# Optimization experiments

Hardware: AMD Instinct MI355X
Metric: run time of the kernel (lower is better)

The kernel has to match this reference:

```python
import jax, jax.numpy as jnp
import numpy as np

DIM = 2048
MLP_MULT = 4
NUM_EXPERTS = 8
EXPERT_INTER = MLP_MULT * DIM // NUM_EXPERTS  # 1024
B, S = 4, 2048


def setup_inputs() -> dict:
    key = jax.random.key(0)
    k1, k2, k3, k4 = jax.random.split(key, 4)
    x = jax.random.normal(k1, (B, S, DIM), dtype=jnp.float32)
    expert_ids = jax.random.randint(k2, (B, S), 0, NUM_EXPERTS, dtype=jnp.int64)
    # kaiming-uniform-ish scale for gate_up; down_proj random (zeros in orig init
    # would make output trivially zero, unhelpful for a correctness baseline)
    bound_gu = float(np.sqrt(1.0 / DIM))
    gate_up_proj = jax.random.uniform(k3, (NUM_EXPERTS, DIM, 2 * EXPERT_INTER),
                                      dtype=jnp.float32, minval=-bound_gu, maxval=bound_gu)
    bound_dn = float(np.sqrt(1.0 / EXPERT_INTER))
    down_proj = jax.random.uniform(k4, (NUM_EXPERTS, EXPERT_INTER, DIM),
                                   dtype=jnp.float32, minval=-bound_dn, maxval=bound_dn)
    return {"x": x, "expert_ids": expert_ids,
            "gate_up_proj": gate_up_proj, "down_proj": down_proj}


def reference(x, expert_ids, gate_up_proj, down_proj):
    Bb, Ss, D = x.shape
    E = gate_up_proj.shape[0]
    flat_x = x.reshape(-1, D)            # [T, D], T = B*S
    flat_ids = expert_ids.reshape(-1)    # [T]
    # Same math as the torch loop: full dense per-expert MLP, then mask.
    gu = jnp.einsum('td,edh->eth', flat_x, gate_up_proj)       # [E, T, 2I]
    g, u = jnp.split(gu, 2, axis=-1)                           # [E, T, I] each
    h = jax.nn.silu(g) * u                                     # [E, T, I]
    y = jnp.einsum('eti,eid->etd', h, down_proj)               # [E, T, D]
    mask = (flat_ids[None, :] == jnp.arange(E)[:, None])[..., None]  # [E, T, 1]
    out = jnp.sum(y * mask.astype(y.dtype), axis=0)            # [T, D]
    return out.reshape(Bb, Ss, D)
```

## Files before the change

kernel.cpp:

```cpp
#include <hip/hip_runtime.h>
#include <cstdint>
#include <cstddef>


typedef __attribute__((ext_vector_type(8))) _Float16 half8;
typedef __attribute__((ext_vector_type(4))) float floatx4;

#define AS_G __attribute__((address_space(1)))
#define AS_L __attribute__((address_space(3)))

__device__ __forceinline__ void async_cp16(void* lds, const void* g) {
  __builtin_amdgcn_global_load_lds((const AS_G uint32_t*)g, (AS_L uint32_t*)lds,
                                   16, 0, 0);
}

static constexpr int TTOK = 8192;
static constexpr int DIMK = 2048;
static constexpr int EI = 1024;
static constexpr int NE = 8;
static constexpr int PADT = 9216;
static constexpr int MAXTILES = 80;
static constexpr int NTILE_LAUNCH = 72;

__global__ __launch_bounds__(256) void k_route(const int* __restrict__ ids,
                                               int* __restrict__ perm,
                                               int* __restrict__ te,
                                               int* __restrict__ tr0,
                                               int* __restrict__ tnr,
                                               int* __restrict__ cur) {
  __shared__ int cnt[NE];
  __shared__ int sstart[NE];
  __shared__ int snpad[NE];
  __shared__ int stotal;
  int tid = threadIdx.x;
  if (tid < NE) cnt[tid] = 0;
  __syncthreads();
  for (int t = tid; t < TTOK; t += 256) atomicAdd(&cnt[ids[t]], 1);
  __syncthreads();
  if (tid == 0) {
    int pr = 0, nt = 0;
    for (int e = 0; e < NE; e++) {
      int n = cnt[e];
      sstart[e] = pr;
      cur[e] = pr;
      int padded = ((n + 127) >> 7) << 7;
      snpad[e] = padded - n;
      for (int j = 0; j < n; j += 128) {
        te[nt] = e; tr0[nt] = pr + j; tnr[nt] = min(128, n - j); nt++;
      }
      pr += padded;
    }
    stotal = pr;
    for (; nt < MAXTILES; nt++) { te[nt] = 0; tr0[nt] = 0; tnr[nt] = 0; }
  }
  __syncthreads();
  for (int e = 0; e < NE; e++) {
    int base = sstart[e] + cnt[e];
    for (int i = tid; i < snpad[e]; i += 256) perm[base + i] = 0;
  }
  for (int i = stotal + tid; i < PADT; i += 256) perm[i] = 0;
}

__global__ __launch_bounds__(256) void k_scatter(const int* __restrict__ ids,
                                                 int* __restrict__ cur,
                                                 int* __restrict__ perm) {
  __shared__ int bcnt[NE], bbase[NE], bloc[NE];
  int tid = threadIdx.x;
  int t = blockIdx.x * 256 + tid;
  if (tid < NE) { bcnt[tid] = 0; bloc[tid] = 0; }
  __syncthreads();
  int e = ids[t];
  atomicAdd(&bcnt[e], 1);
  __syncthreads();
  if (tid < NE && bcnt[tid] > 0) bbase[tid] = atomicAdd(&cur[tid], bcnt[tid]);
  __syncthreads();
  int off = atomicAdd(&bloc[e], 1);
  perm[bbase[e] + off] = t;
}

template <int K, int N>
__device__ __forceinline__ void transpose_tile(const float* __restrict__ src,
                                               _Float16* __restrict__ dst,
                                               float (*tile)[67], int e,
                                               int n0, int k0, int tid) {
  const float* s = src + (size_t)e * K * N;
  _Float16* d = dst + (size_t)e * N * K;
  int kk = tid >> 4;
  int nn = (tid & 15) * 4;
#pragma unroll
  for (int i = 0; i < 4; i++) {
    float4 v = *(const float4*)(s + (size_t)(k0 + kk + i * 16) * N + n0 + nn);
    tile[kk + i * 16][nn + 0] = v.x;
    tile[kk + i * 16][nn + 1] = v.y;
    tile[kk + i * 16][nn + 2] = v.z;
    tile[kk + i * 16][nn + 3] = v.w;
  }
  __syncthreads();
  int nrow = tid >> 3;
  int k8 = (tid & 7) * 8;
#pragma unroll
  for (int i = 0; i < 2; i++) {
    int n = nrow + i * 32;
    half8 o;
#pragma unroll
    for (int j = 0; j < 8; j++) o[j] = (_Float16)tile[k8 + j][n];
    *(half8*)(d + (size_t)(n0 + n) * K + k0 + k8) = o;
  }
}

__global__ __launch_bounds__(256) void k_prep(const float* __restrict__ gup,
                                              _Float16* __restrict__ wt1,
                                              const float* __restrict__ x,
                                              const int* __restrict__ perm,
                                              _Float16* __restrict__ xg) {
  __shared__ float tile[64][67];
  int b = blockIdx.x;
  int tid = threadIdx.x;
  if (b < 8192) {
    int e = b >> 10;
    int r = b & 1023;
    transpose_tile<DIMK, DIMK>(gup, wt1, tile, e, (r & 31) * 64, (r >> 5) * 64,
                               tid);
  } else {
    int row = b - 8192;
    int tok = perm[row];
    int c = tid * 8;
    const float* s = x + (size_t)tok * DIMK + c;
    float4 a = *(const float4*)s;
    float4 bb = *(const float4*)(s + 4);
    half8 o;
    o[0] = (_Float16)a.x; o[1] = (_Float16)a.y;
    o[2] = (_Float16)a.z; o[3] = (_Float16)a.w;
    o[4] = (_Float16)bb.x; o[5] = (_Float16)bb.y;
    o[6] = (_Float16)bb.z; o[7] = (_Float16)bb.w;
    *(half8*)(xg + (size_t)row * DIMK + c) = o;
  }
}

__global__ __launch_bounds__(256) void k_t2(const float* __restrict__ dwn,
                                            _Float16* __restrict__ wt2) {
  __shared__ float tile[64][67];
  transpose_tile<EI, DIMK>(dwn, wt2, tile, blockIdx.z, blockIdx.x * 64,
                           blockIdx.y * 64, threadIdx.x);
}

__global__ __launch_bounds__(256) void k_gateup(
    const _Float16* __restrict__ xg, const _Float16* __restrict__ wt1,
    const int* __restrict__ te, const int* __restrict__ tr0,
    const int* __restrict__ tnr, _Float16* __restrict__ hbuf) {
  int tile = blockIdx.y;
  int nr = tnr[tile];
  if (nr == 0) return;
  int e = te[tile], r0 = tr0[tile];
  int col = blockIdx.x * 64;
  int tid = threadIdx.x;

  __shared__ __align__(16) _Float16 As[128 * 64];
  __shared__ __align__(16) _Float16 Bg[64 * 64];
  __shared__ __align__(16) _Float16 Bu[64 * 64];

  int an = tid >> 2;
  int aq = (tid & 3) ^ ((tid >> 3) & 3);
  const _Float16* ap0 = xg + (size_t)(r0 + an) * DIMK + aq * 8;
  const _Float16* ap1 = ap0 + (size_t)64 * DIMK;
  _Float16* al0 = As + (size_t)tid * 8;
  _Float16* al1 = As + 2048 + (size_t)tid * 8;
  const _Float16* bgp =
      wt1 + (size_t)e * DIMK * DIMK + (size_t)(col + an) * DIMK + aq * 8;
  const _Float16* bup = bgp + (size_t)EI * DIMK;
  _Float16* bgl = Bg + (size_t)tid * 8;
  _Float16* bul = Bu + (size_t)tid * 8;

  int wave = tid >> 6, lane = tid & 63;
  int wm = (wave & 1) * 64, wn = (wave >> 1) * 32;
  int lm = lane & 15, lq = lane >> 4;
  int aoff[4], boff[2];
#pragma unroll
  for (int i = 0; i < 4; i++) {
    int r = wm + i * 16 + lm;
    aoff[i] = (r * 4 + (lq ^ ((r >> 1) & 3))) * 8;
  }
#pragma unroll
  for (int j = 0; j < 2; j++) {
    int n = wn + j * 16 + lm;
    boff[j] = (n * 4 + (lq ^ ((n >> 1) & 3))) * 8;
  }

  floatx4 accg[4][2], accu[4][2];
#pragma unroll
  for (int i = 0; i < 4; i++)
#pragma unroll
    for (int j = 0; j < 2; j++) {
      accg[i][j] = (floatx4)0.0f;
      accu[i][j] = (floatx4)0.0f;
    }

  for (int k0 = 0; k0 < DIMK; k0 += 64) {
    async_cp16(al0, ap0 + k0);
    async_cp16(al1, ap1 + k0);
    async_cp16(bgl, bgp + k0);
    async_cp16(bul, bup + k0);
    async_cp16(al0 + 4096, ap0 + k0 + 32);
    async_cp16(al1 + 4096, ap1 + k0 + 32);
    async_cp16(bgl + 2048, bgp + k0 + 32);
    async_cp16(bul + 2048, bup + k0 + 32);
    __syncthreads();
#pragma unroll
    for (int s = 0; s < 2; s++) {
      const _Float16* Ab = As + s * 4096;
      const _Float16* Bgb = Bg + s * 2048;
      const _Float16* Bub = Bu + s * 2048;
      half8 af[4], bgf[2], buf_[2];
#pragma unroll
      for (int i = 0; i < 4; i++) af[i] = *(const half8*)(Ab + aoff[i]);
#pragma unroll
      for (int j = 0; j < 2; j++) {
        bgf[j] = *(const half8*)(Bgb + boff[j]);
        buf_[j] = *(const half8*)(Bub + boff[j]);
      }
#pragma unroll
      for (int i = 0; i < 4; i++)
#pragma unroll
        for (int j = 0; j < 2; j++) {
          accg[i][j] = __builtin_amdgcn_mfma_f32_16x16x32_f16(
              af[i], bgf[j], accg[i][j], 0, 0, 0);
          accu[i][j] = __builtin_amdgcn_mfma_f32_16x16x32_f16(
              af[i], buf_[j], accu[i][j], 0, 0, 0);
        }
    }
    __syncthreads();
  }

#pragma unroll
  for (int i = 0; i < 4; i++) {
    int rbase = wm + i * 16 + lq * 4;
#pragma unroll
    for (int j = 0; j < 2; j++) {
      int c = col + wn + j * 16 + lm;
#pragma unroll
      for (int rr = 0; rr < 4; rr++) {
        float g = accg[i][j][rr];
        float u = accu[i][j][rr];
        float h = g / (1.0f + __expf(-g)) * u;
        hbuf[(size_t)(r0 + rbase + rr) * EI + c] = (_Float16)h;
      }
    }
  }
}

__global__ __launch_bounds__(256) void k_down(
    const _Float16* __restrict__ hbuf, const _Float16* __restrict__ wt2,
    const int* __restrict__ perm, const int* __restrict__ te,
    const int* __restrict__ tr0, const int* __restrict__ tnr,
    float* __restrict__ out) {
  int tile = blockIdx.y;
  int nr = tnr[tile];
  if (nr == 0) return;
  int e = te[tile], r0 = tr0[tile];
  int col = blockIdx.x * 128;
  int tid = threadIdx.x;

  __shared__ __align__(16) _Float16 As[128 * 64];
  __shared__ __align__(16) _Float16 Bs[128 * 64];

  int an = tid >> 2;
  int aq = (tid & 3) ^ ((tid >> 3) & 3);
  const _Float16* ap0 = hbuf + (size_t)(r0 + an) * EI + aq * 8;
  const _Float16* ap1 = ap0 + (size_t)64 * EI;
  _Float16* al0 = As + (size_t)tid * 8;
  _Float16* al1 = As + 2048 + (size_t)tid * 8;
  const _Float16* wte = wt2 + (size_t)e * DIMK * EI;
  const _Float16* bp0 = wte + (size_t)(col + an) * EI + aq * 8;
  const _Float16* bp1 = bp0 + (size_t)64 * EI;
  _Float16* bl0 = Bs + (size_t)tid * 8;
  _Float16* bl1 = Bs + 2048 + (size_t)tid * 8;

  int wave = tid >> 6, lane = tid & 63;
  int wm = (wave & 1) * 64, wn = (wave >> 1) * 64;
  int lm = lane & 15, lq = lane >> 4;
  int aoff[4], boff[4];
#pragma unroll
  for (int i = 0; i < 4; i++) {
    int r = wm + i * 16 + lm;
    aoff[i] = (r * 4 + (lq ^ ((r >> 1) & 3))) * 8;
    int n = wn + i * 16 + lm;
    boff[i] = (n * 4 + (lq ^ ((n >> 1) & 3))) * 8;
  }

  floatx4 acc[4][4];
#pragma unroll
  for (int i = 0; i < 4; i++)
#pragma unroll
    for (int j = 0; j < 4; j++) acc[i][j] = (floatx4)0.0f;

  for (int k0 = 0; k0 < EI; k0 += 64) {
    async_cp16(al0, ap0 + k0);
    async_cp16(al1, ap1 + k0);
    async_cp16(bl0, bp0 + k0);
    async_cp16(bl1, bp1 + k0);
    async_cp16(al0 + 4096, ap0 + k0 + 32);
    async_cp16(al1 + 4096, ap1 + k0 + 32);
    async_cp16(bl0 + 4096, bp0 + k0 + 32);
    async_cp16(bl1 + 4096, bp1 + k0 + 32);
    __syncthreads();
#pragma unroll
    for (int s = 0; s < 2; s++) {
      const _Float16* Ab = As + s * 4096;
      const _Float16* Bb = Bs + s * 4096;
      half8 af[4], bf[4];
#pragma unroll
      for (int i = 0; i < 4; i++) {
        af[i] = *(const half8*)(Ab + aoff[i]);
        bf[i] = *(const half8*)(Bb + boff[i]);
      }
#pragma unroll
      for (int i = 0; i < 4; i++)
#pragma unroll
        for (int j = 0; j < 4; j++)
          acc[i][j] = __builtin_amdgcn_mfma_f32_16x16x32_f16(af[i], bf[j],
                                                             acc[i][j], 0, 0, 0);
    }
    __syncthreads();
  }

#pragma unroll
  for (int i = 0; i < 4; i++) {
    int rbase = wm + i * 16 + lq * 4;
#pragma unroll
    for (int rr = 0; rr < 4; rr++) {
      int r = rbase + rr;
      if (r < nr) {
        int tok = perm[r0 + r];
        float* orow = out + (size_t)tok * DIMK + col;
#pragma unroll
        for (int j = 0; j < 4; j++) orow[wn + j * 16 + lm] = acc[i][j][rr];
      }
    }
  }
}

extern "C" void kernel_launch(void* const* d_in, const int* in_sizes, int n_in,
                              void* d_out, int out_size, void* d_ws,
                              size_t ws_size, hipStream_t stream) {
  const float* x = (const float*)d_in[0];
  const int* ids = (const int*)d_in[1];
  const float* gup = (const float*)d_in[2];
  const float* dwn = (const float*)d_in[3];
  float* out = (float*)d_out;
  char* ws = (char*)d_ws;

  int* perm = (int*)ws;
  int* te = (int*)(ws + 36864);
  int* tr0 = (int*)(ws + 36864 + 512);
  int* tnr = (int*)(ws + 36864 + 1024);
  int* cur = (int*)(ws + 36864 + 1536);
  _Float16* wt1 = (_Float16*)(ws + 65536);
  _Float16* hbuf = (_Float16*)(ws + 65536 + 67108864);
  _Float16* xg = (_Float16*)(ws + 65536 + 67108864 + 18874368);
  _Float16* wt2 = wt1;

  k_route<<<dim3(1), dim3(256), 0, stream>>>(ids, perm, te, tr0, tnr, cur);
  k_scatter<<<dim3(32), dim3(256), 0, stream>>>(ids, cur, perm);
  k_prep<<<dim3(8192 + PADT), dim3(256), 0, stream>>>(gup, wt1, x, perm, xg);
  k_gateup<<<dim3(16, NTILE_LAUNCH), dim3(256), 0, stream>>>(
      xg, wt1, te, tr0, tnr, hbuf);
  k_t2<<<dim3(32, 16, 8), dim3(256), 0, stream>>>(dwn, wt2);
  k_down<<<dim3(16, NTILE_LAUNCH), dim3(256), 0, stream>>>(
      hbuf, wt2, perm, te, tr0, tnr, out);
}
```

Baseline: 494.7 us.

## Double-buffer LDS tiles and swizzle block-to-tile mapping in both expert GEMMs

Both the gate/up and down-projection GEMM kernels now keep two LDS stages and issue the async global-to-LDS copies for the next K slice before computing on the current one. This is meant to hide global load latency behind MFMA work. Block indices are also flattened and permuted so consecutive hardware block IDs (modulo 8) spread across tiles, which is meant to improve L2 reuse of expert weights across chiplets. The cost is doubled LDS per block, which may reduce occupancy.

```diff
diff --git a/kernel.cpp b/kernel.cpp
--- a/kernel.cpp
+++ b/kernel.cpp
@@ -148,28 +148,26 @@
     const _Float16* __restrict__ xg, const _Float16* __restrict__ wt1,
     const int* __restrict__ te, const int* __restrict__ tr0,
     const int* __restrict__ tnr, _Float16* __restrict__ hbuf) {
-  int tile = blockIdx.y;
+  int flat = blockIdx.y * 16 + blockIdx.x;
+  int swz = (flat & 7) * (NTILE_LAUNCH * 16 / 8) + (flat >> 3);
+  int tile = swz >> 4;
   int nr = tnr[tile];
   if (nr == 0) return;
   int e = te[tile], r0 = tr0[tile];
-  int col = blockIdx.x * 64;
-  int tid = threadIdx.x;
-
-  __shared__ __align__(16) _Float16 As[128 * 64];
-  __shared__ __align__(16) _Float16 Bg[64 * 64];
-  __shared__ __align__(16) _Float16 Bu[64 * 64];
+  int col = (swz & 15) * 64;
+  int tid = threadIdx.x;
+
+  __shared__ __align__(16) _Float16 As[2][128 * 64];
+  __shared__ __align__(16) _Float16 Bg[2][64 * 64];
+  __shared__ __align__(16) _Float16 Bu[2][64 * 64];
 
   int an = tid >> 2;
   int aq = (tid & 3) ^ ((tid >> 3) & 3);
   const _Float16* ap0 = xg + (size_t)(r0 + an) * DIMK + aq * 8;
   const _Float16* ap1 = ap0 + (size_t)64 * DIMK;
-  _Float16* al0 = As + (size_t)tid * 8;
-  _Float16* al1 = As + 2048 + (size_t)tid * 8;
   const _Float16* bgp =
       wt1 + (size_t)e * DIMK * DIMK + (size_t)(col + an) * DIMK + aq * 8;
   const _Float16* bup = bgp + (size_t)EI * DIMK;
-  _Float16* bgl = Bg + (size_t)tid * 8;
-  _Float16* bul = Bu + (size_t)tid * 8;
 
   int wave = tid >> 6, lane = tid & 63;
   int wm = (wave & 1) * 64, wn = (wave >> 1) * 32;
@@ -195,21 +193,31 @@
       accu[i][j] = (floatx4)0.0f;
     }
 
-  for (int k0 = 0; k0 < DIMK; k0 += 64) {
-    async_cp16(al0, ap0 + k0);
-    async_cp16(al1, ap1 + k0);
-    async_cp16(bgl, bgp + k0);
-    async_cp16(bul, bup + k0);
-    async_cp16(al0 + 4096, ap0 + k0 + 32);
-    async_cp16(al1 + 4096, ap1 + k0 + 32);
-    async_cp16(bgl + 2048, bgp + k0 + 32);
-    async_cp16(bul + 2048, bup + k0 + 32);
-    __syncthreads();
+  auto stage = [&](int p, int k0) {
+    _Float16* a = As[p] + (size_t)tid * 8;
+    _Float16* g = Bg[p] + (size_t)tid * 8;
+    _Float16* u = Bu[p] + (size_t)tid * 8;
+    async_cp16(a, ap0 + k0);
+    async_cp16(a + 2048, ap1 + k0);
+    async_cp16(g, bgp + k0);
+    async_cp16(u, bup + k0);
+    async_cp16(a + 4096, ap0 + k0 + 32);
+    async_cp16(a + 6144, ap1 + k0 + 32);
+    async_cp16(g + 2048, bgp + k0 + 32);
+    async_cp16(u + 2048, bup + k0 + 32);
+  };
+
+  stage(0, 0);
+  __syncthreads();
+
+  int p = 0;
+  for (int k0 = 0; k0 < DIMK; k0 += 64, p ^= 1) {
+    if (k0 + 64 < DIMK) stage(p ^ 1, k0 + 64);
 #pragma unroll
     for (int s = 0; s < 2; s++) {
-      const _Float16* Ab = As + s * 4096;
-      const _Float16* Bgb = Bg + s * 2048;
-      const _Float16* Bub = Bu + s * 2048;
+      const _Float16* Ab = As[p] + s * 4096;
+      const _Float16* Bgb = Bg[p] + s * 2048;
+      const _Float16* Bub = Bu[p] + s * 2048;
       half8 af[4], bgf[2], buf_[2];
 #pragma unroll
       for (int i = 0; i < 4; i++) af[i] = *(const half8*)(Ab + aoff[i]);
@@ -253,27 +261,25 @@
     const int* __restrict__ perm, const int* __restrict__ te,
     const int* __restrict__ tr0, const int* __restrict__ tnr,
     float* __restrict__ out) {
-  int tile = blockIdx.y;
+  int flat = blockIdx.y * 16 + blockIdx.x;
+  int swz = (flat & 7) * (NTILE_LAUNCH * 16 / 8) + (flat >> 3);
+  int tile = swz >> 4;
   int nr = tnr[tile];
   if (nr == 0) return;
   int e = te[tile], r0 = tr0[tile];
-  int col = blockIdx.x * 128;
-  int tid = threadIdx.x;
-
-  __shared__ __align__(16) _Float16 As[128 * 64];
-  __shared__ __align__(16) _Float16 Bs[128 * 64];
+  int col = (swz & 15) * 128;
+  int tid = threadIdx.x;
+
+  __shared__ __align__(16) _Float16 As[2][128 * 64];
+  __shared__ __align__(16) _Float16 Bs[2][128 * 64];
 
   int an = tid >> 2;
   int aq = (tid & 3) ^ ((tid >> 3) & 3);
   const _Float16* ap0 = hbuf + (size_t)(r0 + an) * EI + aq * 8;
   const _Float16* ap1 = ap0 + (size_t)64 * EI;
-  _Float16* al0 = As + (size_t)tid * 8;
-  _Float16* al1 = As + 2048 + (size_t)tid * 8;
   const _Float16* wte = wt2 + (size_t)e * DIMK * EI;
   const _Float16* bp0 = wte + (size_t)(col + an) * EI + aq * 8;
   const _Float16* bp1 = bp0 + (size_t)64 * EI;
-  _Float16* bl0 = Bs + (size_t)tid * 8;
-  _Float16* bl1 = Bs + 2048 + (size_t)tid * 8;
 
   int wave = tid >> 6, lane = tid & 63;
   int wm = (wave & 1) * 64, wn = (wave >> 1) * 64;
@@ -293,20 +299,29 @@
 #pragma unroll
     for (int j = 0; j < 4; j++) acc[i][j] = (floatx4)0.0f;
 
-  for (int k0 = 0; k0 < EI; k0 += 64) {
-    async_cp16(al0, ap0 + k0);
-    async_cp16(al1, ap1 + k0);
-    async_cp16(bl0, bp0 + k0);
-    async_cp16(bl1, bp1 + k0);
-    async_cp16(al0 + 4096, ap0 + k0 + 32);
-    async_cp16(al1 + 4096, ap1 + k0 + 32);
-    async_cp16(bl0 + 4096, bp0 + k0 + 32);
-    async_cp16(bl1 + 4096, bp1 + k0 + 32);
-    __syncthreads();
+  auto stage = [&](int p, int k0) {
+    _Float16* a = As[p] + (size_t)tid * 8;
+    _Float16* b = Bs[p] + (size_t)tid * 8;
+    async_cp16(a, ap0 + k0);
+    async_cp16(a + 2048, ap1 + k0);
+    async_cp16(b, bp0 + k0);
+    async_cp16(b + 2048, bp1 + k0);
+    async_cp16(a + 4096, ap0 + k0 + 32);
+    async_cp16(a + 6144, ap1 + k0 + 32);
+    async_cp16(b + 4096, bp0 + k0 + 32);
+    async_cp16(b + 6144, bp1 + k0 + 32);
+  };
+
+  stage(0, 0);
+  __syncthreads();
+
+  int p = 0;
+  for (int k0 = 0; k0 < EI; k0 += 64, p ^= 1) {
+    if (k0 + 64 < EI) stage(p ^ 1, k0 + 64);
 #pragma unroll
     for (int s = 0; s < 2; s++) {
-      const _Float16* Ab = As + s * 4096;
-      const _Float16* Bb = Bs + s * 4096;
+      const _Float16* Ab = As[p] + s * 4096;
+      const _Float16* Bb = Bs[p] + s * 4096;
       half8 af[4], bf[4];
 #pragma unroll
       for (int i = 0; i < 4; i++) {
```

Measured after the change: 500.1 us. No clear change (+1.1%).

## Enlarge MoE GEMM tiles, double-buffer LDS, and swizzle block order

Applied to the files above, without the earlier changes.

Both expert GEMM kernels now compute 128x256 output tiles per block instead of 128x128 (gate-up) and 128x128 (down), halving the grid. The K loop stages half-K slices into two LDS buffers so the next async copy overlaps MFMA work on the current one, with one barrier per half-step. Block indices are remapped so consecutive blocks walk different tiles of the same column block, aimed at better L2 reuse of expert weights. The larger accumulator set (128 floats per lane) raises register pressure, and the bigger tile leaves fewer blocks to fill the CUs.

```diff
diff --git a/kernel.cpp b/kernel.cpp
--- a/kernel.cpp
+++ b/kernel.cpp
@@ -144,196 +144,203 @@
                            blockIdx.y * 64, threadIdx.x);
 }
 
-__global__ __launch_bounds__(256) void k_gateup(
+__global__ __launch_bounds__(256, 2) void k_gu(
     const _Float16* __restrict__ xg, const _Float16* __restrict__ wt1,
     const int* __restrict__ te, const int* __restrict__ tr0,
     const int* __restrict__ tnr, _Float16* __restrict__ hbuf) {
-  int tile = blockIdx.y;
+  int flat = blockIdx.y * 8 + blockIdx.x;
+  int swz = (flat & 7) * NTILE_LAUNCH + (flat >> 3);
+  int tile = swz >> 3, cb = swz & 7;
   int nr = tnr[tile];
   if (nr == 0) return;
   int e = te[tile], r0 = tr0[tile];
-  int col = blockIdx.x * 64;
-  int tid = threadIdx.x;
-
-  __shared__ __align__(16) _Float16 As[128 * 64];
-  __shared__ __align__(16) _Float16 Bg[64 * 64];
-  __shared__ __align__(16) _Float16 Bu[64 * 64];
+  int tid = threadIdx.x;
+
+  __shared__ __align__(16) _Float16 As[2][4096];
+  __shared__ __align__(16) _Float16 Bs[2][8192];
 
   int an = tid >> 2;
-  int aq = (tid & 3) ^ ((tid >> 3) & 3);
-  const _Float16* ap0 = xg + (size_t)(r0 + an) * DIMK + aq * 8;
-  const _Float16* ap1 = ap0 + (size_t)64 * DIMK;
-  _Float16* al0 = As + (size_t)tid * 8;
-  _Float16* al1 = As + 2048 + (size_t)tid * 8;
-  const _Float16* bgp =
-      wt1 + (size_t)e * DIMK * DIMK + (size_t)(col + an) * DIMK + aq * 8;
-  const _Float16* bup = bgp + (size_t)EI * DIMK;
-  _Float16* bgl = Bg + (size_t)tid * 8;
-  _Float16* bul = Bu + (size_t)tid * 8;
+  int aq = (tid & 3) ^ ((an >> 1) & 3);
+  const _Float16* a0 = xg + (size_t)(r0 + an) * DIMK + aq * 8;
+  const _Float16* a1 = a0 + (size_t)64 * DIMK;
+  const _Float16* wte = wt1 + (size_t)e * DIMK * DIMK;
+  const _Float16* g0 = wte + (size_t)(cb * 128 + an) * DIMK + aq * 8;
+  const _Float16* g1 = g0 + (size_t)64 * DIMK;
+  const _Float16* u0 = wte + (size_t)(EI + cb * 128 + an) * DIMK + aq * 8;
+  const _Float16* u1 = u0 + (size_t)64 * DIMK;
+
+  auto stage = [&](int p, int k0) {
+    _Float16* la = &As[p][(size_t)tid * 8];
+    _Float16* lb = &Bs[p][(size_t)tid * 8];
+    async_cp16(la, a0 + k0);
+    async_cp16(la + 2048, a1 + k0);
+    async_cp16(lb, g0 + k0);
+    async_cp16(lb + 2048, g1 + k0);
+    async_cp16(lb + 4096, u0 + k0);
+    async_cp16(lb + 6144, u1 + k0);
+  };
 
   int wave = tid >> 6, lane = tid & 63;
-  int wm = (wave & 1) * 64, wn = (wave >> 1) * 32;
+  int wm = (wave >> 1) * 64;
+  int wn = (wave & 1) * 64;
   int lm = lane & 15, lq = lane >> 4;
-  int aoff[4], boff[2];
+  int aoff[4], boff[8];
 #pragma unroll
   for (int i = 0; i < 4; i++) {
     int r = wm + i * 16 + lm;
     aoff[i] = (r * 4 + (lq ^ ((r >> 1) & 3))) * 8;
   }
 #pragma unroll
-  for (int j = 0; j < 2; j++) {
-    int n = wn + j * 16 + lm;
-    boff[j] = (n * 4 + (lq ^ ((n >> 1) & 3))) * 8;
-  }
-
-  floatx4 accg[4][2], accu[4][2];
+  for (int j = 0; j < 4; j++) {
+    int brg = wn + j * 16 + lm;
+    boff[j] = (brg * 4 + (lq ^ ((brg >> 1) & 3))) * 8;
+    int bru = 128 + wn + j * 16 + lm;
+    boff[j + 4] = (bru * 4 + (lq ^ ((bru >> 1) & 3))) * 8;
+  }
+
+  floatx4 acc[4][8];
 #pragma unroll
   for (int i = 0; i < 4; i++)
 #pragma unroll
-    for (int j = 0; j < 2; j++) {
-      accg[i][j] = (floatx4)0.0f;
-      accu[i][j] = (floatx4)0.0f;
-    }
-
+    for (int j = 0; j < 8; j++) acc[i][j] = (floatx4)0.0f;
+
+  auto compute = [&](int p) {
+    half8 af[4], bf[8];
+#pragma unroll
+    for (int i = 0; i < 4; i++) af[i] = *(const half8*)(&As[p][0] + aoff[i]);
+#pragma unroll
+    for (int j = 0; j < 8; j++) bf[j] = *(const half8*)(&Bs[p][0] + boff[j]);
+#pragma unroll
+    for (int i = 0; i < 4; i++)
+#pragma unroll
+      for (int j = 0; j < 8; j++)
+        acc[i][j] = __builtin_amdgcn_mfma_f32_16x16x32_f16(af[i], bf[j],
+                                                           acc[i][j], 0, 0, 0);
+  };
+
+  stage(0, 0);
+  __syncthreads();
   for (int k0 = 0; k0 < DIMK; k0 += 64) {
-    async_cp16(al0, ap0 + k0);
-    async_cp16(al1, ap1 + k0);
-    async_cp16(bgl, bgp + k0);
-    async_cp16(bul, bup + k0);
-    async_cp16(al0 + 4096, ap0 + k0 + 32);
-    async_cp16(al1 + 4096, ap1 + k0 + 32);
-    async_cp16(bgl + 2048, bgp + k0 + 32);
-    async_cp16(bul + 2048, bup + k0 + 32);
+    stage(1, k0 + 32);
+    compute(0);
     __syncthreads();
-#pragma unroll
-    for (int s = 0; s < 2; s++) {
-      const _Float16* Ab = As + s * 4096;
-      const _Float16* Bgb = Bg + s * 2048;
-      const _Float16* Bub = Bu + s * 2048;
-      half8 af[4], bgf[2], buf_[2];
-#pragma unroll
-      for (int i = 0; i < 4; i++) af[i] = *(const half8*)(Ab + aoff[i]);
-#pragma unroll
-      for (int j = 0; j < 2; j++) {
-        bgf[j] = *(const half8*)(Bgb + boff[j]);
-        buf_[j] = *(const half8*)(Bub + boff[j]);
-      }
-#pragma unroll
-      for (int i = 0; i < 4; i++)
-#pragma unroll
-        for (int j = 0; j < 2; j++) {
-          accg[i][j] = __builtin_amdgcn_mfma_f32_16x16x32_f16(
-              af[i], bgf[j], accg[i][j], 0, 0, 0);
-          accu[i][j] = __builtin_amdgcn_mfma_f32_16x16x32_f16(
-              af[i], buf_[j], accu[i][j], 0, 0, 0);
-        }
-    }
+    if (k0 + 64 < DIMK) stage(0, k0 + 64);
+    compute(1);
     __syncthreads();
   }
 
 #pragma unroll
   for (int i = 0; i < 4; i++) {
-    int rbase = wm + i * 16 + lq * 4;
-#pragma unroll
-    for (int j = 0; j < 2; j++) {
-      int c = col + wn + j * 16 + lm;
+    int rb = wm + i * 16 + lq * 4;
+#pragma unroll
+    for (int j = 0; j < 4; j++) {
+      int c = cb * 128 + wn + j * 16 + lm;
 #pragma unroll
       for (int rr = 0; rr < 4; rr++) {
-        float g = accg[i][j][rr];
-        float u = accu[i][j][rr];
+        float g = acc[i][j][rr];
+        float u = acc[i][j + 4][rr];
         float h = g / (1.0f + __expf(-g)) * u;
-        hbuf[(size_t)(r0 + rbase + rr) * EI + c] = (_Float16)h;
+        hbuf[(size_t)(r0 + rb + rr) * EI + c] = (_Float16)h;
       }
     }
   }
 }
 
-__global__ __launch_bounds__(256) void k_down(
+__global__ __launch_bounds__(256, 2) void k_dn(
     const _Float16* __restrict__ hbuf, const _Float16* __restrict__ wt2,
     const int* __restrict__ perm, const int* __restrict__ te,
     const int* __restrict__ tr0, const int* __restrict__ tnr,
     float* __restrict__ out) {
-  int tile = blockIdx.y;
+  int flat = blockIdx.y * 8 + blockIdx.x;
+  int swz = (flat & 7) * NTILE_LAUNCH + (flat >> 3);
+  int tile = swz >> 3, cb = swz & 7;
   int nr = tnr[tile];
   if (nr == 0) return;
   int e = te[tile], r0 = tr0[tile];
-  int col = blockIdx.x * 128;
-  int tid = threadIdx.x;
-
-  __shared__ __align__(16) _Float16 As[128 * 64];
-  __shared__ __align__(16) _Float16 Bs[128 * 64];
+  int tid = threadIdx.x;
+
+  __shared__ __align__(16) _Float16 As[2][4096];
+  __shared__ __align__(16) _Float16 Bs[2][8192];
 
   int an = tid >> 2;
-  int aq = (tid & 3) ^ ((tid >> 3) & 3);
-  const _Float16* ap0 = hbuf + (size_t)(r0 + an) * EI + aq * 8;
-  const _Float16* ap1 = ap0 + (size_t)64 * EI;
-  _Float16* al0 = As + (size_t)tid * 8;
-  _Float16* al1 = As + 2048 + (size_t)tid * 8;
+  int aq = (tid & 3) ^ ((an >> 1) & 3);
+  const _Float16* a0 = hbuf + (size_t)(r0 + an) * EI + aq * 8;
+  const _Float16* a1 = a0 + (size_t)64 * EI;
   const _Float16* wte = wt2 + (size_t)e * DIMK * EI;
-  const _Float16* bp0 = wte + (size_t)(col + an) * EI + aq * 8;
-  const _Float16* bp1 = bp0 + (size_t)64 * EI;
-  _Float16* bl0 = Bs + (size_t)tid * 8;
-  _Float16* bl1 = Bs + 2048 + (size_t)tid * 8;
+  const _Float16* b0 = wte + (size_t)(cb * 256 + an) * EI + aq * 8;
+  const _Float16* b1 = b0 + (size_t)64 * EI;
+  const _Float16* b2 = b0 + (size_t)128 * EI;
+  const _Float16* b3 = b0 + (size_t)192 * EI;
+
+  auto stage = [&](int p, int k0) {
+    _Float16* la = &As[p][(size_t)tid * 8];
+    _Float16* lb = &Bs[p][(size_t)tid * 8];
+    async_cp16(la, a0 + k0);
+    async_cp16(la + 2048, a1 + k0);
+    async_cp16(lb, b0 + k0);
+    async_cp16(lb + 2048, b1 + k0);
+    async_cp16(lb + 4096, b2 + k0);
+    async_cp16(lb + 6144, b3 + k0);
+  };
 
   int wave = tid >> 6, lane = tid & 63;
-  int wm = (wave & 1) * 64, wn = (wave >> 1) * 64;
+  int wm = (wave >> 1) * 64;
+  int wn = (wave & 1) * 128;
   int lm = lane & 15, lq = lane >> 4;
-  int aoff[4], boff[4];
+  int aoff[4], boff[8];
 #pragma unroll
   for (int i = 0; i < 4; i++) {
     int r = wm + i * 16 + lm;
     aoff[i] = (r * 4 + (lq ^ ((r >> 1) & 3))) * 8;
-    int n = wn + i * 16 + lm;
-    boff[i] = (n * 4 + (lq ^ ((n >> 1) & 3))) * 8;
-  }
-
-  floatx4 acc[4][4];
+  }
+#pragma unroll
+  for (int j = 0; j < 8; j++) {
+    int br = wn + j * 16 + lm;
+    boff[j] = (br * 4 + (lq ^ ((br >> 1) & 3))) * 8;
+  }
+
+  floatx4 acc[4][8];
 #pragma unroll
   for (int i = 0; i < 4; i++)
 #pragma unroll
-    for (int j = 0; j < 4; j++) acc[i][j] = (floatx4)0.0f;
-
+    for (int j = 0; j < 8; j++) acc[i][j] = (floatx4)0.0f;
+
+  auto compute = [&](int p) {
+    half8 af[4], bf[8];
+#pragma unroll
+    for (int i = 0; i < 4; i++) af[i] = *(const half8*)(&As[p][0] + aoff[i]);
+#pragma unroll
+    for (int j = 0; j < 8; j++) bf[j] = *(const half8*)(&Bs[p][0] + boff[j]);
+#pragma unroll
+    for (int i = 0; i < 4; i++)
+#pragma unroll
+      for (int j = 0; j < 8; j++)
+        acc[i][j] = __builtin_amdgcn_mfma_f32_16x16x32_f16(af[i], bf[j],
+                                                           acc[i][j], 0, 0, 0);
+  };
+
+  stage(0, 0);
+  __syncthreads();
   for (int k0 = 0; k0 < EI; k0 += 64) {
-    async_cp16(al0, ap0 + k0);
-    async_cp16(al1, ap1 + k0);
-    async_cp16(bl0, bp0 + k0);
-    async_cp16(bl1, bp1 + k0);
-    async_cp16(al0 + 4096, ap0 + k0 + 32);
-    async_cp16(al1 + 4096, ap1 + k0 + 32);
-    async_cp16(bl0 + 4096, bp0 + k0 + 32);
-    async_cp16(bl1 + 4096, bp1 + k0 + 32);
+    stage(1, k0 + 32);
+    compute(0);
     __syncthreads();
-#pragma unroll
-    for (int s = 0; s < 2; s++) {
-      const _Float16* Ab = As + s * 4096;
-      const _Float16* Bb = Bs + s * 4096;
-      half8 af[4], bf[4];
-#pragma unroll
-      for (int i = 0; i < 4; i++) {
-        af[i] = *(const half8*)(Ab + aoff[i]);
-        bf[i] = *(const half8*)(Bb + boff[i]);
-      }
-#pragma unroll
-      for (int i = 0; i < 4; i++)
-#pragma unroll
-        for (int j = 0; j < 4; j++)
-          acc[i][j] = __builtin_amdgcn_mfma_f32_16x16x32_f16(af[i], bf[j],
-                                                             acc[i][j], 0, 0, 0);
-    }
+    if (k0 + 64 < EI) stage(0, k0 + 64);
+    compute(1);
     __syncthreads();
   }
 
 #pragma unroll
   for (int i = 0; i < 4; i++) {
-    int rbase = wm + i * 16 + lq * 4;
+    int rb = wm + i * 16 + lq * 4;
 #pragma unroll
     for (int rr = 0; rr < 4; rr++) {
-      int r = rbase + rr;
+      int r = rb + rr;
       if (r < nr) {
         int tok = perm[r0 + r];
-        float* orow = out + (size_t)tok * DIMK + col;
-#pragma unroll
-        for (int j = 0; j < 4; j++) orow[wn + j * 16 + lm] = acc[i][j][rr];
+        float* orow = out + (size_t)tok * DIMK + cb * 256;
+#pragma unroll
+        for (int j = 0; j < 8; j++) orow[wn + j * 16 + lm] = acc[i][j][rr];
       }
     }
   }
@@ -362,9 +369,9 @@
   k_route<<<dim3(1), dim3(256), 0, stream>>>(ids, perm, te, tr0, tnr, cur);
   k_scatter<<<dim3(32), dim3(256), 0, stream>>>(ids, cur, perm);
   k_prep<<<dim3(8192 + PADT), dim3(256), 0, stream>>>(gup, wt1, x, perm, xg);
-  k_gateup<<<dim3(16, NTILE_LAUNCH), dim3(256), 0, stream>>>(
+  k_gu<<<dim3(8, NTILE_LAUNCH), dim3(256), 0, stream>>>(
       xg, wt1, te, tr0, tnr, hbuf);
   k_t2<<<dim3(32, 16, 8), dim3(256), 0, stream>>>(dwn, wt2);
-  k_down<<<dim3(16, NTILE_LAUNCH), dim3(256), 0, stream>>>(
+  k_dn<<<dim3(8, NTILE_LAUNCH), dim3(256), 0, stream>>>(
       hbuf, wt2, perm, te, tr0, tnr, out);
 }
```

New measurement: 521.7 us. +5.5%, slower.
